# Kernel optimization log

Hardware: AMD Instinct MI355X
Metric: run time of the kernel (lower is better)

Reference implementation:

```python
import jax, jax.numpy as jnp
import numpy as np

B, N, D, D_OUT = 8, 2048, 256, 256
LN_EPS = 1e-5
LRELU_SLOPE = 0.01


def setup_inputs() -> dict:
    key = jax.random.key(0)
    ks = jax.random.split(key, 11)
    s_in = 1.0 / np.sqrt(D)
    s_out = 1.0 / np.sqrt(D)
    return {
        "x_local": jax.random.normal(ks[0], (B, N, D), dtype=jnp.float32),
        "Wq": jax.random.uniform(ks[1], (D, D), jnp.float32, -s_in, s_in),
        "bq": jax.random.uniform(ks[2], (D,), jnp.float32, -s_in, s_in),
        "Wk": jax.random.uniform(ks[3], (D, D), jnp.float32, -s_in, s_in),
        "bk": jax.random.uniform(ks[4], (D,), jnp.float32, -s_in, s_in),
        "Wv": jax.random.uniform(ks[5], (D, D), jnp.float32, -s_in, s_in),
        "bv": jax.random.uniform(ks[6], (D,), jnp.float32, -s_in, s_in),
        "Wo": jax.random.uniform(ks[7], (D_OUT, D), jnp.float32, -s_out, s_out),
        "bo": jax.random.uniform(ks[8], (D_OUT,), jnp.float32, -s_out, s_out),
        "ln_gamma": jnp.ones((D_OUT,), jnp.float32),
        "ln_beta": jnp.zeros((D_OUT,), jnp.float32),
    }


def reference(x_local, Wq, bq, Wk, bk, Wv, bv, Wo, bo, ln_gamma, ln_beta):
    # Linear layers (torch convention: y = x @ W.T + b)
    Q = jnp.einsum("bnd,ed->bne", x_local, Wq) + bq
    K = jnp.einsum("bnd,ed->bne", x_local, Wk) + bk
    V = jnp.einsum("bnd,ed->bne", x_local, Wv) + bv
    # Unscaled attention (source applies no 1/sqrt(d))
    scores = jnp.einsum("bnd,bmd->bnm", Q, K)          # [B, N, N]
    attn = jax.nn.softmax(scores, axis=-1)
    loc = jnp.einsum("bnm,bmd->bnd", attn, V)           # [B, N, D]
    # fc_out: Linear -> LayerNorm -> LeakyReLU
    h = jnp.einsum("bnd,ed->bne", loc, Wo) + bo          # [B, N, D_OUT]
    mu = jnp.mean(h, axis=-1, keepdims=True)
    var = jnp.mean(jnp.square(h - mu), axis=-1, keepdims=True)
    hn = (h - mu) / jnp.sqrt(var + LN_EPS) * ln_gamma + ln_beta
    return jnp.where(hn >= 0, hn, LRELU_SLOPE * hn)
```

## Files before the change

kernel.cpp:

```cpp
#include <hip/hip_runtime.h>

typedef unsigned short u16;
typedef __attribute__((ext_vector_type(8))) _Float16 f16x8;
typedef __attribute__((ext_vector_type(4))) float f32x4;

#define MFMA_F16 __builtin_amdgcn_mfma_f32_16x16x32_f16

static __device__ __forceinline__ u16 f2h(float f) {
    return __builtin_bit_cast(u16, (_Float16)f);
}
static __device__ __forceinline__ ushort4 f4_to_h4(const float4 v) {
    ushort4 r;
    r.x = f2h(v.x); r.y = f2h(v.y); r.z = f2h(v.z); r.w = f2h(v.w);
    return r;
}
static __device__ __forceinline__ void gl16(const u16* g, u16* l) {
    __builtin_amdgcn_global_load_lds(
        (__attribute__((address_space(1))) void*)(g),
        (__attribute__((address_space(3))) void*)(l),
        16, 0, 0);
}

__global__ __launch_bounds__(256) void prep_w(
    const float* __restrict__ wq, const float* __restrict__ wk,
    const float* __restrict__ wv, const float* __restrict__ wo,
    const float* __restrict__ x,
    u16* __restrict__ w4, u16* __restrict__ xh)
{
    const int tid = blockIdx.x * 256 + threadIdx.x;
    {
        const float* src = (tid < 16384) ? wq : (tid < 32768) ? wk
                         : (tid < 49152) ? wv : wo;
        ((ushort4*)w4)[tid] = f4_to_h4(((const float4*)src)[tid & 16383]);
    }
#pragma unroll
    for (int i = 0; i < 16; ++i) {
        const int j = i * 65536 + tid;
        ((ushort4*)xh)[j] = f4_to_h4(((const float4*)x)[j]);
    }
}

__global__ __launch_bounds__(256, 3) void proj_qkv(
    const u16* __restrict__ Xh, const u16* __restrict__ w4,
    const float* __restrict__ bq, const float* __restrict__ bk,
    const float* __restrict__ bv,
    u16* __restrict__ Qh, u16* __restrict__ Kh, u16* __restrict__ Vt)
{
    const int z = blockIdx.y;
    const u16* __restrict__ W     = w4 + z * 65536;
    const float* __restrict__ bias = (z == 0) ? bq : (z == 1) ? bk : bv;

    const int m0   = blockIdx.x * 64;
    const int t    = threadIdx.x;
    const int w    = t >> 6;
    const int lane = t & 63;
    const int quad = lane >> 4;
    const int l16  = lane & 15;

    __shared__ __align__(16) u16 smem[20480];

    const int xrow = t >> 2, xpp = t & 3;
    const unsigned xsrc = (unsigned)((m0 + xrow) * 256
                        + ((xpp ^ ((xrow >> 1) & 3)) * 8));
    unsigned wsrc[4];
#pragma unroll
    for (int i = 0; i < 4; ++i) {
        const int j = i * 256 + t;
        const int row = j >> 2, p = j & 3;
        wsrc[i] = (unsigned)(row * 256 + ((p ^ ((row >> 1) & 3)) * 8));
    }

#define PSTAGE(bufsel, kc_) do {                                             \
        u16* B_ = smem + (bufsel) * 10240;                                   \
        gl16(Xh + xsrc + (unsigned)(kc_) * 32, B_ + w * 512);                \
        _Pragma("unroll")                                                    \
        for (int i_ = 0; i_ < 4; ++i_)                                       \
            gl16(W + wsrc[i_] + (unsigned)(kc_) * 32,                        \
                 B_ + 2048 + i_ * 2048 + w * 512);                           \
    } while (0)

    f32x4 acc[16];
#pragma unroll
    for (int i = 0; i < 16; ++i) acc[i] = f32x4{0.f, 0.f, 0.f, 0.f};

    const int rp = (quad ^ ((l16 >> 1) & 3)) * 8;

    PSTAGE(0, 0);

    for (int kc = 0; kc < 8; ++kc) {
        asm volatile("s_waitcnt vmcnt(0)" ::: "memory");
        __builtin_amdgcn_s_barrier();
        __builtin_amdgcn_sched_barrier(0);
        if (kc + 1 < 8) PSTAGE((kc + 1) & 1, kc + 1);
        __builtin_amdgcn_sched_barrier(0);

        const u16* Xb = smem + (kc & 1) * 10240;
        const u16* Wb = Xb + 2048;

        const f16x8 af = *(const f16x8*)&Xb[(w * 16 + l16) * 32 + rp];
        __builtin_amdgcn_s_setprio(1);
#pragma unroll
        for (int nt = 0; nt < 16; ++nt) {
            const f16x8 bf = *(const f16x8*)&Wb[(nt * 16 + l16) * 32 + rp];
            acc[nt] = MFMA_F16(af, bf, acc[nt], 0, 0, 0);
        }
        __builtin_amdgcn_s_setprio(0);
    }
#undef PSTAGE

    __syncthreads();

    if (z < 2) {
        u16* __restrict__ Y = (z == 0) ? Qh : Kh;
#pragma unroll
        for (int nt = 0; nt < 16; ++nt) {
            const int col = nt * 16 + l16;
            const float bb = bias[col];
#pragma unroll
            for (int r = 0; r < 4; ++r)
                smem[(w * 16 + quad * 4 + r) * 264 + col] = f2h(acc[nt][r] + bb);
        }
        __syncthreads();
#pragma unroll
        for (int i = 0; i < 8; ++i) {
            const int ch = i * 256 + t;
            const int row = ch >> 5, cg = ch & 31;
            *(int4*)&Y[(size_t)(m0 + row) * 256 + cg * 8] =
                *(const int4*)&smem[row * 264 + cg * 8];
        }
    } else {
        const int b  = m0 >> 11;
        const int n0 = m0 & 2047;
#pragma unroll
        for (int nt = 0; nt < 16; ++nt) {
            const int col = nt * 16 + l16;
            const float bb = bias[col];
            ushort4 h4;
            h4.x = f2h(acc[nt][0] + bb);
            h4.y = f2h(acc[nt][1] + bb);
            h4.z = f2h(acc[nt][2] + bb);
            h4.w = f2h(acc[nt][3] + bb);
            *(ushort4*)&smem[col * 72 + w * 16 + quad * 4] = h4;
        }
        __syncthreads();
#pragma unroll
        for (int i = 0; i < 8; ++i) {
            const int ch = i * 256 + t;
            const int row = ch >> 3, cg = ch & 7;
            *(int4*)&Vt[(size_t)b * 524288 + (size_t)row * 2048 + n0 + cg * 8] =
                *(const int4*)&smem[row * 72 + cg * 8];
        }
    }
}

__global__ __launch_bounds__(256, 2) void attn(
    const u16* __restrict__ Qh, const u16* __restrict__ Kg,
    const u16* __restrict__ Vt, u16* __restrict__ Op, float* __restrict__ lmp)
{
    const int nz = gridDim.z;
    const int z  = blockIdx.z;
    const int ntiles = 32;
    const int tile0  = ntiles * z;

    const int b  = blockIdx.y;
    const int q0 = blockIdx.x * 64;
    const int t    = threadIdx.x;
    const int w    = t >> 6;
    const int lane = t & 63;
    const int quad = lane >> 4;
    const int l16  = lane & 15;

    __shared__ __align__(16) u16 smem[32768];
    u16* Os = smem;

    f16x8 qf[8];
    {
        const size_t qrow = (size_t)(b * 2048 + q0 + w * 16 + l16) * 256;
#pragma unroll
        for (int kc = 0; kc < 8; ++kc)
            qf[kc] = *(const f16x8*)&Qh[qrow + kc * 32 + quad * 8];
    }

    unsigned kgb[4], vgb[4];
#pragma unroll
    for (int i = 0; i < 4; ++i) {
        const int j  = w * 4 + i;
        const int r  = 2 * j + (lane >> 5);
        const int pr = ((r >> 2) & 3) * 8 + (r >> 4) * 4 + (r & 3);
        const int c  = lane & 31;
        kgb[i] = (unsigned)((b * 2048 + pr) * 256 + ((c ^ (r & 7)) * 8));
        const int rp2 = 8 * j + (lane >> 3);
        const int c8 = lane & 7;
        const int d  = 2 * rp2 + (c8 >> 2);
        const int a  = (c8 & 3) ^ (rp2 & 3);
        vgb[i] = (unsigned)(b * 524288 + d * 2048 + a * 8);
    }

#define STAGE(bufsel, kt_) do {                                              \
        u16* Kb_ = smem + (bufsel) * 16384;                                  \
        u16* Vb_ = Kb_ + 8192;                                               \
        _Pragma("unroll")                                                    \
        for (int i_ = 0; i_ < 4; ++i_) {                                     \
            gl16(Kg + kgb[i_] + (unsigned)(kt_) * 256,                       \
                 Kb_ + (w * 4 + i_) * 512);                                  \
            gl16(Vt + vgb[i_] + (unsigned)(kt_),                             \
                 Vb_ + (w * 4 + i_) * 512);                                  \
        }                                                                    \
    } while (0)

    f32x4 O[16];
#pragma unroll
    for (int i = 0; i < 16; ++i) O[i] = f32x4{0.f, 0.f, 0.f, 0.f};
    float mrow = -1e30f, lrow = 0.f;

    const int vbase = (l16 >> 1) * 64 + (l16 & 1) * 32
                    + ((quad ^ ((l16 >> 1) & 3)) * 8);

    STAGE(0, tile0 * 32);

    for (int it = 0; it < ntiles; ++it) {
        asm volatile("s_waitcnt vmcnt(0)" ::: "memory");
        __builtin_amdgcn_s_barrier();
        __builtin_amdgcn_sched_barrier(0);
        if (it + 1 < ntiles) STAGE((it + 1) & 1, (tile0 + it + 1) * 32);
        __builtin_amdgcn_sched_barrier(0);

        const u16* Kc = smem + (it & 1) * 16384;
        const u16* Vc = Kc + 8192;

        f32x4 S[2];
        S[0] = f32x4{0.f, 0.f, 0.f, 0.f};
        S[1] = f32x4{0.f, 0.f, 0.f, 0.f};
        __builtin_amdgcn_s_setprio(1);
#pragma unroll
        for (int kc = 0; kc < 8; ++kc) {
#pragma unroll
            for (int kn = 0; kn < 2; ++kn) {
                const int r2 = kn * 16 + l16;
                const f16x8 kf = *(const f16x8*)
                    &Kc[r2 * 256 + (((kc * 4 + quad) ^ (l16 & 7)) * 8)];
                S[kn] = MFMA_F16(kf, qf[kc], S[kn], 0, 0, 0);
            }
        }
        __builtin_amdgcn_s_setprio(0);

        float mt = fmaxf(fmaxf(fmaxf(S[0][0], S[0][1]), fmaxf(S[0][2], S[0][3])),
                         fmaxf(fmaxf(S[1][0], S[1][1]), fmaxf(S[1][2], S[1][3])));
        mt = fmaxf(mt, __shfl_xor(mt, 16));
        mt = fmaxf(mt, __shfl_xor(mt, 32));
        if (__any(mt - mrow > 8.f)) {
            const float mnew = fmaxf(mrow, mt);
            const float a = __expf(mrow - mnew);
            lrow *= a;
#pragma unroll
            for (int dv = 0; dv < 16; ++dv)
#pragma unroll
                for (int r = 0; r < 4; ++r) O[dv][r] *= a;
            mrow = mnew;
        }
        f16x8 pfv;
        float s = 0.f;
#pragma unroll
        for (int kn = 0; kn < 2; ++kn)
#pragma unroll
            for (int r = 0; r < 4; ++r) {
                const float e = __expf(S[kn][r] - mrow);
                s += e;
                pfv[kn * 4 + r] = (_Float16)e;
            }
        s += __shfl_xor(s, 16);
        s += __shfl_xor(s, 32);
        lrow += s;

        __builtin_amdgcn_s_setprio(1);
#pragma unroll
        for (int dvt = 0; dvt < 16; ++dvt) {
            const f16x8 vf = *(const f16x8*)&Vc[dvt * 512 + vbase];
            O[dvt] = MFMA_F16(vf, pfv, O[dvt], 0, 0, 0);
        }
        __builtin_amdgcn_s_setprio(0);
    }
#undef STAGE

    __syncthreads();
    {
        const float rl = 1.0f / lrow;
#pragma unroll
        for (int dvt = 0; dvt < 16; ++dvt) {
            ushort4 h4;
            h4.x = f2h(O[dvt][0] * rl);
            h4.y = f2h(O[dvt][1] * rl);
            h4.z = f2h(O[dvt][2] * rl);
            h4.w = f2h(O[dvt][3] * rl);
            *(ushort4*)&Os[(w * 16 + l16) * 264 + dvt * 16 + quad * 4] = h4;
        }
        if (quad == 0) {
            const int grow = b * 2048 + q0 + w * 16 + l16;
            lmp[z * 16384 + grow]        = lrow;
            lmp[(nz + z) * 16384 + grow] = mrow;
        }
    }
    __syncthreads();

    u16* __restrict__ Oz = Op + (size_t)z * 4194304;
    {
        const int row = t >> 2;
#pragma unroll
        for (int i = 0; i < 8; ++i) {
            const int chunk = (t & 3) * 8 + i;
            *(int4*)&Oz[(size_t)(b * 2048 + q0 + row) * 256 + chunk * 8] =
                *(const int4*)&Os[row * 264 + chunk * 8];
        }
    }
}

__global__ __launch_bounds__(256, 2) void outproj_ln(
    const u16* __restrict__ Op, const float* __restrict__ lmp,
    const u16* __restrict__ Woh, const float* __restrict__ bo,
    const float* __restrict__ gamma, const float* __restrict__ beta,
    float* __restrict__ out)
{
    const int m0   = blockIdx.x * 32;
    const int t    = threadIdx.x;
    const int w    = t >> 6;
    const int rw   = w & 1;
    const int cw   = w >> 1;
    const int lane = t & 63;
    const int quad = lane >> 4;
    const int l16  = lane & 15;

    __shared__ __align__(16) u16 Ls[32 * 40];
    __shared__ __align__(16) u16 Ws[256 * 40];
    __shared__ _Float16 wls[2][32];
    __shared__ float part[2][16][2][2];

    if (t < 32) {
        const float l0 = lmp[m0 + t],          l1 = lmp[16384 + m0 + t];
        const float mm0 = lmp[32768 + m0 + t], mm1 = lmp[49152 + m0 + t];
        const float mm = fmaxf(mm0, mm1);
        const float u0 = l0 * __expf(mm0 - mm);
        const float u1 = l1 * __expf(mm1 - mm);
        const float inv = 1.0f / (u0 + u1);
        wls[0][t] = (_Float16)(u0 * inv);
        wls[1][t] = (_Float16)(u1 * inv);
    }
    __syncthreads();

    f32x4 acc[8];
#pragma unroll
    for (int i = 0; i < 8; ++i) acc[i] = f32x4{0.f, 0.f, 0.f, 0.f};

    for (int kc = 0; kc < 8; ++kc) {
        if (t < 128) {
            const int row = t >> 2, cg = t & 3;
            const size_t off = (size_t)(m0 + row) * 256 + kc * 32 + cg * 8;
            const f16x8 o0 = __builtin_bit_cast(f16x8, *(const int4*)&Op[off]);
            const f16x8 o1 = __builtin_bit_cast(f16x8, *(const int4*)&Op[4194304 + off]);
            const _Float16 w0 = wls[0][row], w1 = wls[1][row];
            f16x8 lw;
#pragma unroll
            for (int j = 0; j < 8; ++j) lw[j] = o0[j] * w0 + o1[j] * w1;
            *(int4*)&Ls[row * 40 + cg * 8] = __builtin_bit_cast(int4, lw);
        }
#pragma unroll
        for (int i = 0; i < 4; ++i) {
            const int ch = i * 256 + t;
            const int row = ch >> 2, cg = ch & 3;
            *(int4*)&Ws[row * 40 + cg * 8] =
                *(const int4*)&Woh[(size_t)row * 256 + kc * 32 + cg * 8];
        }
        __syncthreads();

        const f16x8 af = *(const f16x8*)&Ls[(rw * 16 + l16) * 40 + quad * 8];
#pragma unroll
        for (int nt = 0; nt < 8; ++nt) {
            const f16x8 bf = *(const f16x8*)&Ws[((cw * 8 + nt) * 16 + l16) * 40 + quad * 8];
            acc[nt] = MFMA_F16(af, bf, acc[nt], 0, 0, 0);
        }
        __syncthreads();
    }

    float g[8], bt[8], bb[8];
#pragma unroll
    for (int nt = 0; nt < 8; ++nt) {
        const int col = cw * 128 + nt * 16 + l16;
        bb[nt] = bo[col]; g[nt] = gamma[col]; bt[nt] = beta[col];
    }

    float shv[4], sh2v[4];
#pragma unroll
    for (int r = 0; r < 4; ++r) {
        float sh = 0.f, sh2 = 0.f;
#pragma unroll
        for (int nt = 0; nt < 8; ++nt) {
            const float h = acc[nt][r] + bb[nt];
            sh  += h;
            sh2 += h * h;
        }
        sh  += __shfl_xor(sh, 1);  sh  += __shfl_xor(sh, 2);
        sh  += __shfl_xor(sh, 4);  sh  += __shfl_xor(sh, 8);
        sh2 += __shfl_xor(sh2, 1); sh2 += __shfl_xor(sh2, 2);
        sh2 += __shfl_xor(sh2, 4); sh2 += __shfl_xor(sh2, 8);
        shv[r] = sh; sh2v[r] = sh2;
    }
    if (l16 == 0) {
#pragma unroll
        for (int r = 0; r < 4; ++r) {
            part[rw][quad * 4 + r][cw][0] = shv[r];
            part[rw][quad * 4 + r][cw][1] = sh2v[r];
        }
    }
    __syncthreads();

#pragma unroll
    for (int r = 0; r < 4; ++r) {
        const float sh  = shv[r]  + part[rw][quad * 4 + r][cw ^ 1][0];
        const float sh2 = sh2v[r] + part[rw][quad * 4 + r][cw ^ 1][1];
        const float mu  = sh * (1.f / 256.f);
        const float var = fmaxf(sh2 * (1.f / 256.f) - mu * mu, 0.f);
        const float rs  = rsqrtf(var + 1e-5f);
        const size_t row = (size_t)(m0 + rw * 16 + quad * 4 + r) * 256;
#pragma unroll
        for (int nt = 0; nt < 8; ++nt) {
            const float hn = (acc[nt][r] + bb[nt] - mu) * rs * g[nt] + bt[nt];
            out[row + cw * 128 + nt * 16 + l16] = (hn >= 0.f) ? hn : 0.01f * hn;
        }
    }
}

extern "C" void kernel_launch(void* const* d_in, const int* in_sizes, int n_in,
                              void* d_out, int out_size, void* d_ws, size_t ws_size,
                              hipStream_t stream)
{
    const float* x  = (const float*)d_in[0];
    const float* Wq = (const float*)d_in[1];
    const float* bq = (const float*)d_in[2];
    const float* Wk = (const float*)d_in[3];
    const float* bk = (const float*)d_in[4];
    const float* Wv = (const float*)d_in[5];
    const float* bv = (const float*)d_in[6];
    const float* Wo = (const float*)d_in[7];
    const float* bo = (const float*)d_in[8];
    const float* gm = (const float*)d_in[9];
    const float* bt = (const float*)d_in[10];
    float* out = (float*)d_out;

    u16* W4 = (u16*)d_ws;
    u16* Qh = W4 + 262144;
    u16* Kh = Qh + 4194304;
    u16* Vt = Kh + 4194304;
    u16* Op = Vt + 4194304;
    float* lmp = (float*)(Op + 2 * 4194304);
    u16* Woh = W4 + 196608;
    u16* Xh  = (u16*)d_out;

    prep_w     <<<256,            256, 0, stream>>>(Wq, Wk, Wv, Wo, x, W4, Xh);
    proj_qkv   <<<dim3(256, 3),   256, 0, stream>>>(Xh, W4, bq, bk, bv, Qh, Kh, Vt);
    attn       <<<dim3(32, 8, 2), 256, 0, stream>>>(Qh, Kh, Vt, Op, lmp);
    outproj_ln <<<512,            256, 0, stream>>>(Op, lmp, Woh, bo, gm, bt, out);
}
```

Before: 167.3 us.

## Widen attention blocks to 128 queries and split keys four ways

The attention kernel now runs 512-thread blocks covering 128 query rows, so each staged K/V tile feeds twice as many waves. The key range is split into four chunks instead of two. The extra partial outputs and their softmax statistics go into reused scratch space (the output buffer and the weight workspace). The out-projection kernel now merges four partials with log-sum-exp weights. The aim is to cut redundant K/V global and LDS traffic per query while keeping enough blocks in flight. In exchange, the launch bounds ask for four 512-thread blocks per CU, which could force heavy register limits or spills, and it adds more partial-output traffic.

Measured after the change: 185.2 us. 10.7% more time.

```diff
diff --git a/kernel.cpp b/kernel.cpp
--- a/kernel.cpp
+++ b/kernel.cpp
@@ -153,24 +153,25 @@
     }
 }
 
-__global__ __launch_bounds__(256, 2) void attn(
+__global__ __launch_bounds__(512, 4) void attn(
     const u16* __restrict__ Qh, const u16* __restrict__ Kg,
-    const u16* __restrict__ Vt, u16* __restrict__ Op, float* __restrict__ lmp)
+    const u16* __restrict__ Vt, u16* __restrict__ Op,
+    u16* __restrict__ OutS, float* __restrict__ lmpL, float* __restrict__ lmpM)
 {
     const int nz = gridDim.z;
     const int z  = blockIdx.z;
-    const int ntiles = 32;
+    const int ntiles = 64 / nz;
     const int tile0  = ntiles * z;
 
     const int b  = blockIdx.y;
-    const int q0 = blockIdx.x * 64;
+    const int q0 = blockIdx.x * 128;
     const int t    = threadIdx.x;
     const int w    = t >> 6;
     const int lane = t & 63;
     const int quad = lane >> 4;
     const int l16  = lane & 15;
 
-    __shared__ __align__(16) u16 smem[32768];
+    __shared__ __align__(16) u16 smem[34816];
     u16* Os = smem;
 
     f16x8 qf[8];
@@ -181,10 +182,10 @@
             qf[kc] = *(const f16x8*)&Qh[qrow + kc * 32 + quad * 8];
     }
 
-    unsigned kgb[4], vgb[4];
-#pragma unroll
-    for (int i = 0; i < 4; ++i) {
-        const int j  = w * 4 + i;
+    unsigned kgb[2], vgb[2];
+#pragma unroll
+    for (int i = 0; i < 2; ++i) {
+        const int j  = w * 2 + i;
         const int r  = 2 * j + (lane >> 5);
         const int pr = ((r >> 2) & 3) * 8 + (r >> 4) * 4 + (r & 3);
         const int c  = lane & 31;
@@ -200,11 +201,11 @@
         u16* Kb_ = smem + (bufsel) * 16384;                                  \
         u16* Vb_ = Kb_ + 8192;                                               \
         _Pragma("unroll")                                                    \
-        for (int i_ = 0; i_ < 4; ++i_) {                                     \
+        for (int i_ = 0; i_ < 2; ++i_) {                                     \
             gl16(Kg + kgb[i_] + (unsigned)(kt_) * 256,                       \
-                 Kb_ + (w * 4 + i_) * 512);                                  \
+                 Kb_ + (w * 2 + i_) * 512);                                  \
             gl16(Vt + vgb[i_] + (unsigned)(kt_),                             \
-                 Vb_ + (w * 4 + i_) * 512);                                  \
+                 Vb_ + (w * 2 + i_) * 512);                                  \
         }                                                                    \
     } while (0)
 
@@ -296,26 +297,37 @@
         }
         if (quad == 0) {
             const int grow = b * 2048 + q0 + w * 16 + l16;
-            lmp[z * 16384 + grow]        = lrow;
-            lmp[(nz + z) * 16384 + grow] = mrow;
+            lmpL[z * 16384 + grow] = lrow;
+            lmpM[z * 16384 + grow] = mrow;
         }
     }
     __syncthreads();
 
-    u16* __restrict__ Oz = Op + (size_t)z * 4194304;
     {
         const int row = t >> 2;
-#pragma unroll
-        for (int i = 0; i < 8; ++i) {
-            const int chunk = (t & 3) * 8 + i;
-            *(int4*)&Oz[(size_t)(b * 2048 + q0 + row) * 256 + chunk * 8] =
-                *(const int4*)&Os[row * 264 + chunk * 8];
+        if (z < 2) {
+            u16* __restrict__ Oz = Op + (size_t)z * 4194304;
+#pragma unroll
+            for (int i = 0; i < 8; ++i) {
+                const int chunk = (t & 3) * 8 + i;
+                *(int4*)&Oz[(size_t)(b * 2048 + q0 + row) * 256 + chunk * 8] =
+                    *(const int4*)&Os[row * 264 + chunk * 8];
+            }
+        } else {
+            u16* __restrict__ Oz = OutS + (size_t)(z - 2) * 256;
+#pragma unroll
+            for (int i = 0; i < 8; ++i) {
+                const int chunk = (t & 3) * 8 + i;
+                *(int4*)&Oz[(size_t)(b * 2048 + q0 + row) * 512 + chunk * 8] =
+                    *(const int4*)&Os[row * 264 + chunk * 8];
+            }
         }
     }
 }
 
 __global__ __launch_bounds__(256, 2) void outproj_ln(
-    const u16* __restrict__ Op, const float* __restrict__ lmp,
+    const u16* __restrict__ Op, const u16* __restrict__ OutS,
+    const float* __restrict__ lmpL, const float* __restrict__ lmpM,
     const u16* __restrict__ Woh, const float* __restrict__ bo,
     const float* __restrict__ gamma, const float* __restrict__ beta,
     float* __restrict__ out)
@@ -331,18 +343,28 @@
 
     __shared__ __align__(16) u16 Ls[32 * 40];
     __shared__ __align__(16) u16 Ws[256 * 40];
-    __shared__ _Float16 wls[2][32];
+    __shared__ _Float16 wls[4][32];
     __shared__ float part[2][16][2][2];
 
     if (t < 32) {
-        const float l0 = lmp[m0 + t],          l1 = lmp[16384 + m0 + t];
-        const float mm0 = lmp[32768 + m0 + t], mm1 = lmp[49152 + m0 + t];
-        const float mm = fmaxf(mm0, mm1);
-        const float u0 = l0 * __expf(mm0 - mm);
-        const float u1 = l1 * __expf(mm1 - mm);
-        const float inv = 1.0f / (u0 + u1);
+        const float l0 = lmpL[m0 + t];
+        const float l1 = lmpL[16384 + m0 + t];
+        const float l2 = lmpL[32768 + m0 + t];
+        const float l3 = lmpL[49152 + m0 + t];
+        const float m0v = lmpM[m0 + t];
+        const float m1v = lmpM[16384 + m0 + t];
+        const float m2v = lmpM[32768 + m0 + t];
+        const float m3v = lmpM[49152 + m0 + t];
+        const float mm = fmaxf(fmaxf(m0v, m1v), fmaxf(m2v, m3v));
+        const float u0 = l0 * __expf(m0v - mm);
+        const float u1 = l1 * __expf(m1v - mm);
+        const float u2 = l2 * __expf(m2v - mm);
+        const float u3 = l3 * __expf(m3v - mm);
+        const float inv = 1.0f / (u0 + u1 + u2 + u3);
         wls[0][t] = (_Float16)(u0 * inv);
         wls[1][t] = (_Float16)(u1 * inv);
+        wls[2][t] = (_Float16)(u2 * inv);
+        wls[3][t] = (_Float16)(u3 * inv);
     }
     __syncthreads();
 
@@ -353,13 +375,18 @@
     for (int kc = 0; kc < 8; ++kc) {
         if (t < 128) {
             const int row = t >> 2, cg = t & 3;
-            const size_t off = (size_t)(m0 + row) * 256 + kc * 32 + cg * 8;
+            const size_t off  = (size_t)(m0 + row) * 256 + kc * 32 + cg * 8;
+            const size_t offS = (size_t)(m0 + row) * 512 + kc * 32 + cg * 8;
             const f16x8 o0 = __builtin_bit_cast(f16x8, *(const int4*)&Op[off]);
             const f16x8 o1 = __builtin_bit_cast(f16x8, *(const int4*)&Op[4194304 + off]);
+            const f16x8 o2 = __builtin_bit_cast(f16x8, *(const int4*)&OutS[offS]);
+            const f16x8 o3 = __builtin_bit_cast(f16x8, *(const int4*)&OutS[offS + 256]);
             const _Float16 w0 = wls[0][row], w1 = wls[1][row];
+            const _Float16 w2 = wls[2][row], w3 = wls[3][row];
             f16x8 lw;
 #pragma unroll
-            for (int j = 0; j < 8; ++j) lw[j] = o0[j] * w0 + o1[j] * w1;
+            for (int j = 0; j < 8; ++j)
+                lw[j] = o0[j] * w0 + o1[j] * w1 + o2[j] * w2 + o3[j] * w3;
             *(int4*)&Ls[row * 40 + cg * 8] = __builtin_bit_cast(int4, lw);
         }
 #pragma unroll
@@ -450,12 +477,14 @@
     u16* Kh = Qh + 4194304;
     u16* Vt = Kh + 4194304;
     u16* Op = Vt + 4194304;
-    float* lmp = (float*)(Op + 2 * 4194304);
+    float* lmpM = (float*)(Op + 2 * 4194304);
+    float* lmpL = (float*)W4;
     u16* Woh = W4 + 196608;
     u16* Xh  = (u16*)d_out;
+    u16* OutS = (u16*)d_out;
 
     prep_w     <<<256,            256, 0, stream>>>(Wq, Wk, Wv, Wo, x, W4, Xh);
     proj_qkv   <<<dim3(256, 3),   256, 0, stream>>>(Xh, W4, bq, bk, bv, Qh, Kh, Vt);
-    attn       <<<dim3(32, 8, 2), 256, 0, stream>>>(Qh, Kh, Vt, Op, lmp);
-    outproj_ln <<<512,            256, 0, stream>>>(Op, lmp, Woh, bo, gm, bt, out);
-}
+    attn       <<<dim3(16, 8, 4), 512, 0, stream>>>(Qh, Kh, Vt, Op, OutS, lmpL, lmpM);
+    outproj_ln <<<512,            256, 0, stream>>>(Op, OutS, lmpL, lmpM, Woh, bo, gm, bt, out);
+}
```
